# Kernel optimization log

Measured on AMD Instinct MI355X. Metric: run time of the kernel, lower is better.

Reference implementation:

```python
import jax, jax.numpy as jnp
import numpy as np

# NF4 codebook (bitsandbytes values)
NF4_LEVELS = jnp.array([-1.0, -0.6961928009986877, -0.5250730514526367, -0.39491748809814453,
                        -0.28444138169288635, -0.18477343022823334, -0.09105003625154495, 0.0,
                        0.07958029955625534, 0.16093020141124725, 0.24611230194568634,
                        0.33791524171829224, 0.44070982933044434, 0.5626170039176941,
                        0.7229568362236023, 1.0], dtype=jnp.float32)

IN_FEATURES = 4096
OUT_FEATURES = 4096


def setup_inputs() -> dict:
    key = jax.random.key(0)
    k1, k2, k3, k4 = jax.random.split(key, 4)
    x = jax.random.normal(k1, (4, 2048, IN_FEATURES), dtype=jnp.float32)
    # packed uint8 bytes (stored as int32 in [0,256)), shape (O, I//2)
    packed = jax.random.randint(k2, (OUT_FEATURES, IN_FEATURES // 2), 0, 256, dtype=jnp.int32)
    absmax = jax.random.uniform(k3, (OUT_FEATURES,), dtype=jnp.float32) + 1e-3
    bias = jax.random.normal(k4, (OUT_FEATURES,), dtype=jnp.float32)
    return {"x": x, "packed": packed, "absmax": absmax, "bias": bias}


def dequantize_nf4(packed, absmax):
    # packed: (O, I//2) int bytes; high nibble first, then low nibble
    high = (packed >> 4) & 15
    low = packed & 15
    idx = jnp.stack([high, low], axis=2).reshape(packed.shape[0], -1)  # (O, I)
    w = NF4_LEVELS[idx]                    # LUT dequant, (O, I)
    return w * absmax[:, None]             # per-row absmax scaling


def reference(x, packed, absmax, bias):
    # forward: dequantize weight on-the-fly, then F.linear(x, W, bias)
    w = dequantize_nf4(packed, absmax)     # (O, I)
    return jnp.einsum('bsi,oi->bso', x, w) + bias
```

## Files before the change

### kernel.cpp

```cpp
#include <hip/hip_runtime.h>
#include <hip/hip_bf16.h>
#include <stdint.h>

#define M_DIM 8192
#define N_DIM 4096
#define K_DIM 4096

typedef __bf16 bf16_t;
typedef __attribute__((ext_vector_type(8))) __bf16 bf16x8;
typedef __attribute__((ext_vector_type(4))) __bf16 bf16x4;
typedef __attribute__((ext_vector_type(4))) float f32x4;
typedef __attribute__((ext_vector_type(16))) float f32x16;

__constant__ float NF4_LUT[16] = {
    -1.0f, -0.6961928009986877f, -0.5250730514526367f, -0.39491748809814453f,
    -0.28444138169288635f, -0.18477343022823334f, -0.09105003625154495f, 0.0f,
    0.07958029955625534f, 0.16093020141124725f, 0.24611230194568634f,
    0.33791524171829224f, 0.44070982933044434f, 0.5626170039176941f,
    0.7229568362236023f, 1.0f};

__global__ __launch_bounds__(256) void dequant_nf4_kernel(
    const int* __restrict__ packed, const float* __restrict__ absmax,
    bf16_t* __restrict__ W) {
  const int t = blockIdx.x * 256 + threadIdx.x;
  const int row = t >> 9;
  const int c = t & 511;
  const int lane = threadIdx.x & 63;
  const int lutbits = __float_as_int(NF4_LUT[lane & 15]);

  const int4 p = ((const int4*)packed)[t];
  const float am = absmax[row];
  bf16x8 v;
#pragma unroll
  for (int q = 0; q < 4; ++q) {
    const int byte = (q == 0 ? p.x : q == 1 ? p.y : q == 2 ? p.z : p.w) & 255;
    const float hi =
        __int_as_float(__builtin_amdgcn_ds_bpermute(((byte >> 4) & 15) << 2, lutbits));
    const float lo =
        __int_as_float(__builtin_amdgcn_ds_bpermute((byte & 15) << 2, lutbits));
    v[2 * q] = (bf16_t)(hi * am);
    v[2 * q + 1] = (bf16_t)(lo * am);
  }
  *((bf16x8*)&W[(size_t)row * K_DIM + c * 8]) = v;
}

__global__ __launch_bounds__(256) void cvt_bf16_kernel(
    const float* __restrict__ x, bf16_t* __restrict__ y) {
  const int t = blockIdx.x * 256 + threadIdx.x;
  const float4 a = ((const float4*)x)[t];
  bf16x4 v;
  v[0] = (bf16_t)a.x; v[1] = (bf16_t)a.y; v[2] = (bf16_t)a.z; v[3] = (bf16_t)a.w;
  *((bf16x4*)&y[(size_t)t * 4]) = v;
}

#define GLD_LDS16(g, l)                                                     \
  __builtin_amdgcn_global_load_lds(                                        \
      (const __attribute__((address_space(1))) void*)(g),                   \
      (__attribute__((address_space(3))) void*)(l), 16, 0, 0)

#define MFMA32(a, b, c) \
  __builtin_amdgcn_mfma_f32_32x32x16_bf16((a), (b), (c), 0, 0, 0)

#define STAGE_A1(tt, lds)                                    \
  do {                                                       \
    GLD_LDS16(gA1a + (size_t)(tt) * 64, (lds) + dA0);        \
    GLD_LDS16(gA1b + (size_t)(tt) * 64, (lds) + dA0 + 16384);\
  } while (0)
#define STAGE_A2(tt, lds)                                    \
  do {                                                       \
    GLD_LDS16(gA2a + (size_t)(tt) * 64, (lds) + dA0 + 8192); \
    GLD_LDS16(gA2b + (size_t)(tt) * 64, (lds) + dA0 + 24576);\
  } while (0)
#define STAGE_B1(tt, lds)                                    \
  do {                                                       \
    GLD_LDS16(gB1a + (size_t)(tt) * 64, (lds) + dB0);        \
    GLD_LDS16(gB1b + (size_t)(tt) * 64, (lds) + dB0 + 16384);\
  } while (0)
#define STAGE_B2(tt, lds)                                    \
  do {                                                       \
    GLD_LDS16(gB2a + (size_t)(tt) * 64, (lds) + dB0 + 4096); \
    GLD_LDS16(gB2b + (size_t)(tt) * 64, (lds) + dB0 + 20480);\
  } while (0)

#define END_BARRIER()                \
  asm volatile("" ::: "memory");     \
  __builtin_amdgcn_s_barrier();      \
  asm volatile("" ::: "memory")

#define MID_BARRIER()                                   \
  asm volatile("" ::: "memory");                        \
  __builtin_amdgcn_s_barrier();                         \
  asm volatile("s_waitcnt lgkmcnt(0)" ::: "memory");    \
  __builtin_amdgcn_sched_barrier(0)

__global__ __launch_bounds__(512, 2) void gemm_nf4_kernel(
    const bf16_t* __restrict__ A, const bf16_t* __restrict__ B,
    const float* __restrict__ bias, float* __restrict__ C) {
  constexpr int NT = K_DIM / 64;
  __shared__ __align__(16) bf16_t sA[2][256 * 64];
  __shared__ __align__(16) bf16_t sB[2][256 * 64];

  const int tid = threadIdx.x;
  const int wave = tid >> 6, lane = tid & 63;
  const int wm = wave >> 2, wn = wave & 3;
  const int l31 = lane & 31, hi = lane >> 5, l7 = lane & 7;

  const int id = (blockIdx.x & 7) * 64 + (blockIdx.x >> 3);
  const int blockM = (id & 31) * 256;
  const int blockN = (id >> 5) * 256;

  const int rqa = tid >> 3;
  const int cira = ((tid & 7) ^ (rqa & 7)) * 8;
  const bf16_t* gA1a = A + (size_t)(blockM + rqa) * K_DIM + cira;
  const bf16_t* gA1b = gA1a + (size_t)128 * K_DIM;
  const bf16_t* gA2a = gA1a + (size_t)64 * K_DIM;
  const bf16_t* gA2b = gA1a + (size_t)192 * K_DIM;
  const int s0 = tid >> 8, cis = tid & 255;
  const int rqb = cis >> 3;
  const int cirb = ((cis & 7) ^ (rqb & 7)) * 8;
  const bf16_t* gB1a = B + (size_t)(blockN + s0 * 64 + rqb) * K_DIM + cirb;
  const bf16_t* gB1b = gB1a + (size_t)128 * K_DIM;
  const bf16_t* gB2a = gB1a + (size_t)32 * K_DIM;
  const bf16_t* gB2b = gB1a + (size_t)160 * K_DIM;
  const int dA0 = tid * 16;
  const int dB0 = s0 * 8192 + cis * 16;

  const int aBase = (wm * 128 + l31) * 128;
  const int bBase = (wn * 64 + l31) * 128;
  int cOff[4];
#pragma unroll
  for (int ks = 0; ks < 4; ++ks) cOff[ks] = ((ks * 2 + hi) ^ l7) * 16;

  f32x16 acc[4][2];
#pragma unroll
  for (int i = 0; i < 4; ++i)
#pragma unroll
    for (int j = 0; j < 2; ++j) acc[i][j] = (f32x16)(0.0f);

  {
    char* sa0 = (char*)sA[0];
    char* sb0 = (char*)sB[0];
    char* sa1 = (char*)sA[1];
    char* sb1 = (char*)sB[1];
    STAGE_A1(0, sa0);
    STAGE_B1(0, sb0);
    STAGE_A2(0, sa0);
    STAGE_B2(0, sb0);
    STAGE_A1(1, sa1);
    STAGE_B1(1, sb1);
    asm volatile("s_waitcnt vmcnt(4)" ::: "memory");
    __builtin_amdgcn_s_barrier();
    asm volatile("" ::: "memory");
  }

  for (int t = 0; t < NT; ++t) {
    char* sa = (char*)sA[t & 1];
    char* sao = (char*)sA[(t + 1) & 1];
    char* sb = (char*)sB[t & 1];
    char* sbo = (char*)sB[(t + 1) & 1];

    bf16x8 af[2][4], bq[2][4];

#pragma unroll
    for (int mt = 0; mt < 2; ++mt)
#pragma unroll
      for (int ks = 0; ks < 4; ++ks)
        af[mt][ks] = *(const bf16x8*)(sa + aBase + mt * 4096 + cOff[ks]);
#pragma unroll
    for (int nt = 0; nt < 2; ++nt)
#pragma unroll
      for (int ks = 0; ks < 4; ++ks)
        bq[nt][ks] = *(const bf16x8*)(sb + bBase + nt * 4096 + cOff[ks]);
    if (t + 1 < NT) {
      STAGE_A2(t + 1, sao);
      STAGE_B2(t + 1, sbo);
    }
    asm volatile("s_waitcnt lgkmcnt(8)" ::: "memory");
    MID_BARRIER();
    __builtin_amdgcn_s_setprio(1);
#pragma unroll
    for (int ks = 0; ks < 4; ++ks)
#pragma unroll
      for (int mt = 0; mt < 2; ++mt)
#pragma unroll
        for (int nt = 0; nt < 2; ++nt)
          acc[mt][nt] = MFMA32(af[mt][ks], bq[nt][ks], acc[mt][nt]);
    __builtin_amdgcn_s_setprio(0);
    END_BARRIER();

#pragma unroll
    for (int mt = 0; mt < 2; ++mt)
#pragma unroll
      for (int ks = 0; ks < 4; ++ks)
        af[mt][ks] = *(const bf16x8*)(sa + aBase + 8192 + mt * 4096 + cOff[ks]);
    if (t + 2 < NT) {
      STAGE_A1(t + 2, sa);
      STAGE_B1(t + 2, sb);
    }
    MID_BARRIER();
    __builtin_amdgcn_s_setprio(1);
#pragma unroll
    for (int ks = 0; ks < 4; ++ks)
#pragma unroll
      for (int mt = 0; mt < 2; ++mt)
#pragma unroll
        for (int nt = 0; nt < 2; ++nt)
          acc[2 + mt][nt] = MFMA32(af[mt][ks], bq[nt][ks], acc[2 + mt][nt]);
    __builtin_amdgcn_s_setprio(0);
    if (t < NT - 2)
      asm volatile("s_waitcnt vmcnt(4)" ::: "memory");
    else
      asm volatile("s_waitcnt vmcnt(0)" ::: "memory");
    END_BARRIER();
  }

#pragma unroll
  for (int nt = 0; nt < 2; ++nt) {
    const int n = blockN + wn * 64 + nt * 32 + l31;
    const float bv = bias[n];
#pragma unroll
    for (int mt = 0; mt < 4; ++mt) {
      const int mbase = blockM + wm * 128 + mt * 32 + hi * 4;
      f32x16 v = acc[mt][nt];
#pragma unroll
      for (int r = 0; r < 16; ++r) {
        const int m = mbase + (r & 3) + 8 * (r >> 2);
        C[(size_t)m * N_DIM + n] = v[r] + bv;
      }
    }
  }
}

__global__ __launch_bounds__(256) void fallback_kernel(
    const float* __restrict__ x, const int* __restrict__ packed,
    const float* __restrict__ absmax, const float* __restrict__ bias,
    float* __restrict__ out) {
  const int idx = blockIdx.x * 256 + threadIdx.x;
  const int m = idx / N_DIM, n = idx % N_DIM;
  const int* prow = packed + (size_t)n * (K_DIM / 2);
  const float* xr = x + (size_t)m * K_DIM;
  float s = 0.0f;
  for (int p = 0; p < K_DIM / 2; ++p) {
    const int b = prow[p] & 255;
    s += xr[2 * p] * NF4_LUT[(b >> 4) & 15] + xr[2 * p + 1] * NF4_LUT[b & 15];
  }
  out[idx] = s * absmax[n] + bias[n];
}

extern "C" void kernel_launch(void* const* d_in, const int* in_sizes, int n_in,
                              void* d_out, int out_size, void* d_ws,
                              size_t ws_size, hipStream_t stream) {
  const float* x = (const float*)d_in[0];
  const int* packed = (const int*)d_in[1];
  const float* absmax = (const float*)d_in[2];
  const float* bias = (const float*)d_in[3];
  float* out = (float*)d_out;

  const size_t wBytes = (size_t)N_DIM * K_DIM * sizeof(bf16_t);
  const size_t xBytes = (size_t)M_DIM * K_DIM * sizeof(bf16_t);
  if (ws_size < wBytes + xBytes) {
    fallback_kernel<<<dim3((M_DIM * N_DIM) / 256), dim3(256), 0, stream>>>(
        x, packed, absmax, bias, out);
    return;
  }

  bf16_t* W = (bf16_t*)d_ws;
  bf16_t* xb = (bf16_t*)((char*)d_ws + wBytes);

  dequant_nf4_kernel<<<dim3((N_DIM * (K_DIM / 2) / 4) / 256), dim3(256), 0,
                       stream>>>(packed, absmax, W);
  cvt_bf16_kernel<<<dim3((M_DIM * K_DIM / 4) / 256), dim3(256), 0, stream>>>(
      x, xb);
  gemm_nf4_kernel<<<dim3((M_DIM / 256) * (N_DIM / 256)), dim3(512), 0,
                    stream>>>(xb, W, bias, out);
}
```

Measured before the change: 521.4 us.

## Switch GEMM to 16x16x32 MFMA, drop mid barriers, merge prep kernels

The GEMM inner loop now uses 16x16x32 bf16 MFMA tiles with 8x4 accumulators per wave instead of 32x32x16, with new LDS read offsets and epilogue indexing. One of the two block barriers per half-iteration is removed and replaced with an lgkmcnt(0) fence. The dequant and x-conversion kernels are merged into one launch to save a kernel launch. Removing barriers risks races on the double-buffered LDS, and smaller MFMA tiles need more instructions for the same work.

```diff
diff --git a/kernel.cpp b/kernel.cpp
--- a/kernel.cpp
+++ b/kernel.cpp
@@ -10,7 +10,6 @@
 typedef __attribute__((ext_vector_type(8))) __bf16 bf16x8;
 typedef __attribute__((ext_vector_type(4))) __bf16 bf16x4;
 typedef __attribute__((ext_vector_type(4))) float f32x4;
-typedef __attribute__((ext_vector_type(16))) float f32x16;
 
 __constant__ float NF4_LUT[16] = {
     -1.0f, -0.6961928009986877f, -0.5250730514526367f, -0.39491748809814453f,
@@ -19,38 +18,42 @@
     0.33791524171829224f, 0.44070982933044434f, 0.5626170039176941f,
     0.7229568362236023f, 1.0f};
 
-__global__ __launch_bounds__(256) void dequant_nf4_kernel(
+#define DQ_BLOCKS ((N_DIM * (K_DIM / 2) / 4) / 256)
+#define CVT_BLOCKS ((M_DIM * K_DIM / 4) / 256)
+
+__global__ __launch_bounds__(256) void prep_kernel(
     const int* __restrict__ packed, const float* __restrict__ absmax,
-    bf16_t* __restrict__ W) {
-  const int t = blockIdx.x * 256 + threadIdx.x;
-  const int row = t >> 9;
-  const int c = t & 511;
-  const int lane = threadIdx.x & 63;
-  const int lutbits = __float_as_int(NF4_LUT[lane & 15]);
-
-  const int4 p = ((const int4*)packed)[t];
-  const float am = absmax[row];
-  bf16x8 v;
-#pragma unroll
-  for (int q = 0; q < 4; ++q) {
-    const int byte = (q == 0 ? p.x : q == 1 ? p.y : q == 2 ? p.z : p.w) & 255;
-    const float hi =
-        __int_as_float(__builtin_amdgcn_ds_bpermute(((byte >> 4) & 15) << 2, lutbits));
-    const float lo =
-        __int_as_float(__builtin_amdgcn_ds_bpermute((byte & 15) << 2, lutbits));
-    v[2 * q] = (bf16_t)(hi * am);
-    v[2 * q + 1] = (bf16_t)(lo * am);
-  }
-  *((bf16x8*)&W[(size_t)row * K_DIM + c * 8]) = v;
-}
-
-__global__ __launch_bounds__(256) void cvt_bf16_kernel(
-    const float* __restrict__ x, bf16_t* __restrict__ y) {
-  const int t = blockIdx.x * 256 + threadIdx.x;
-  const float4 a = ((const float4*)x)[t];
-  bf16x4 v;
-  v[0] = (bf16_t)a.x; v[1] = (bf16_t)a.y; v[2] = (bf16_t)a.z; v[3] = (bf16_t)a.w;
-  *((bf16x4*)&y[(size_t)t * 4]) = v;
+    bf16_t* __restrict__ W, const float* __restrict__ x,
+    bf16_t* __restrict__ y) {
+  if (blockIdx.x < DQ_BLOCKS) {
+    const int t = blockIdx.x * 256 + threadIdx.x;
+    const int row = t >> 9;
+    const int c = t & 511;
+    const int lane = threadIdx.x & 63;
+    const int lutbits = __float_as_int(NF4_LUT[lane & 15]);
+
+    const int4 p = ((const int4*)packed)[t];
+    const float am = absmax[row];
+    bf16x8 v;
+#pragma unroll
+    for (int q = 0; q < 4; ++q) {
+      const int byte = (q == 0 ? p.x : q == 1 ? p.y : q == 2 ? p.z : p.w) & 255;
+      const float hi = __int_as_float(
+          __builtin_amdgcn_ds_bpermute(((byte >> 4) & 15) << 2, lutbits));
+      const float lo = __int_as_float(
+          __builtin_amdgcn_ds_bpermute((byte & 15) << 2, lutbits));
+      v[2 * q] = (bf16_t)(hi * am);
+      v[2 * q + 1] = (bf16_t)(lo * am);
+    }
+    *((bf16x8*)&W[(size_t)row * K_DIM + c * 8]) = v;
+  } else {
+    const int t = (blockIdx.x - DQ_BLOCKS) * 256 + threadIdx.x;
+    const float4 a = ((const float4*)x)[t];
+    bf16x4 v;
+    v[0] = (bf16_t)a.x; v[1] = (bf16_t)a.y;
+    v[2] = (bf16_t)a.z; v[3] = (bf16_t)a.w;
+    *((bf16x4*)&y[(size_t)t * 4]) = v;
+  }
 }
 
 #define GLD_LDS16(g, l)                                                     \
@@ -58,8 +61,8 @@
       (const __attribute__((address_space(1))) void*)(g),                   \
       (__attribute__((address_space(3))) void*)(l), 16, 0, 0)
 
-#define MFMA32(a, b, c) \
-  __builtin_amdgcn_mfma_f32_32x32x16_bf16((a), (b), (c), 0, 0, 0)
+#define MFMA16(a, b, c) \
+  __builtin_amdgcn_mfma_f32_16x16x32_bf16((a), (b), (c), 0, 0, 0)
 
 #define STAGE_A1(tt, lds)                                    \
   do {                                                       \
@@ -82,14 +85,12 @@
     GLD_LDS16(gB2b + (size_t)(tt) * 64, (lds) + dB0 + 20480);\
   } while (0)
 
-#define END_BARRIER()                \
+#define BARRIER()                    \
   asm volatile("" ::: "memory");     \
   __builtin_amdgcn_s_barrier();      \
   asm volatile("" ::: "memory")
 
-#define MID_BARRIER()                                   \
-  asm volatile("" ::: "memory");                        \
-  __builtin_amdgcn_s_barrier();                         \
+#define LGKM0_FENCE()                                   \
   asm volatile("s_waitcnt lgkmcnt(0)" ::: "memory");    \
   __builtin_amdgcn_sched_barrier(0)
 
@@ -103,7 +104,7 @@
   const int tid = threadIdx.x;
   const int wave = tid >> 6, lane = tid & 63;
   const int wm = wave >> 2, wn = wave & 3;
-  const int l31 = lane & 31, hi = lane >> 5, l7 = lane & 7;
+  const int quad = lane >> 4, l15 = lane & 15, l7 = lane & 7;
 
   const int id = (blockIdx.x & 7) * 64 + (blockIdx.x >> 3);
   const int blockM = (id & 31) * 256;
@@ -125,17 +126,16 @@
   const int dA0 = tid * 16;
   const int dB0 = s0 * 8192 + cis * 16;
 
-  const int aBase = (wm * 128 + l31) * 128;
-  const int bBase = (wn * 64 + l31) * 128;
-  int cOff[4];
-#pragma unroll
-  for (int ks = 0; ks < 4; ++ks) cOff[ks] = ((ks * 2 + hi) ^ l7) * 16;
-
-  f32x16 acc[4][2];
-#pragma unroll
-  for (int i = 0; i < 4; ++i)
-#pragma unroll
-    for (int j = 0; j < 2; ++j) acc[i][j] = (f32x16)(0.0f);
+  const int aBase = (wm * 128 + l15) * 128;
+  const int bBase = (wn * 64 + l15) * 128;
+  const int sl0 = (quad ^ l7) * 16;
+  const int sl1 = ((4 | quad) ^ l7) * 16;
+
+  f32x4 acc[8][4];
+#pragma unroll
+  for (int i = 0; i < 8; ++i)
+#pragma unroll
+    for (int j = 0; j < 4; ++j) acc[i][j] = (f32x4)(0.0f);
 
   {
     char* sa0 = (char*)sA[0];
@@ -159,74 +159,72 @@
     char* sb = (char*)sB[t & 1];
     char* sbo = (char*)sB[(t + 1) & 1];
 
-    bf16x8 af[2][4], bq[2][4];
-
-#pragma unroll
-    for (int mt = 0; mt < 2; ++mt)
-#pragma unroll
-      for (int ks = 0; ks < 4; ++ks)
-        af[mt][ks] = *(const bf16x8*)(sa + aBase + mt * 4096 + cOff[ks]);
-#pragma unroll
-    for (int nt = 0; nt < 2; ++nt)
-#pragma unroll
-      for (int ks = 0; ks < 4; ++ks)
-        bq[nt][ks] = *(const bf16x8*)(sb + bBase + nt * 4096 + cOff[ks]);
+    bf16x8 af[4][2], bq[4][2];
+
+#pragma unroll
+    for (int i = 0; i < 4; ++i) {
+      af[i][0] = *(const bf16x8*)(sa + aBase + i * 2048 + sl0);
+      af[i][1] = *(const bf16x8*)(sa + aBase + i * 2048 + sl1);
+    }
+#pragma unroll
+    for (int j = 0; j < 4; ++j) {
+      bq[j][0] = *(const bf16x8*)(sb + bBase + j * 2048 + sl0);
+      bq[j][1] = *(const bf16x8*)(sb + bBase + j * 2048 + sl1);
+    }
     if (t + 1 < NT) {
       STAGE_A2(t + 1, sao);
       STAGE_B2(t + 1, sbo);
     }
-    asm volatile("s_waitcnt lgkmcnt(8)" ::: "memory");
-    MID_BARRIER();
+    BARRIER();
+    LGKM0_FENCE();
     __builtin_amdgcn_s_setprio(1);
 #pragma unroll
-    for (int ks = 0; ks < 4; ++ks)
-#pragma unroll
-      for (int mt = 0; mt < 2; ++mt)
-#pragma unroll
-        for (int nt = 0; nt < 2; ++nt)
-          acc[mt][nt] = MFMA32(af[mt][ks], bq[nt][ks], acc[mt][nt]);
+    for (int i = 0; i < 4; ++i)
+#pragma unroll
+      for (int j = 0; j < 4; ++j) {
+        acc[i][j] = MFMA16(af[i][0], bq[j][0], acc[i][j]);
+        acc[i][j] = MFMA16(af[i][1], bq[j][1], acc[i][j]);
+      }
     __builtin_amdgcn_s_setprio(0);
-    END_BARRIER();
-
-#pragma unroll
-    for (int mt = 0; mt < 2; ++mt)
-#pragma unroll
-      for (int ks = 0; ks < 4; ++ks)
-        af[mt][ks] = *(const bf16x8*)(sa + aBase + 8192 + mt * 4096 + cOff[ks]);
+
+#pragma unroll
+    for (int i = 0; i < 4; ++i) {
+      af[i][0] = *(const bf16x8*)(sa + aBase + 8192 + i * 2048 + sl0);
+      af[i][1] = *(const bf16x8*)(sa + aBase + 8192 + i * 2048 + sl1);
+    }
     if (t + 2 < NT) {
       STAGE_A1(t + 2, sa);
       STAGE_B1(t + 2, sb);
     }
-    MID_BARRIER();
+    LGKM0_FENCE();
     __builtin_amdgcn_s_setprio(1);
 #pragma unroll
-    for (int ks = 0; ks < 4; ++ks)
-#pragma unroll
-      for (int mt = 0; mt < 2; ++mt)
-#pragma unroll
-        for (int nt = 0; nt < 2; ++nt)
-          acc[2 + mt][nt] = MFMA32(af[mt][ks], bq[nt][ks], acc[2 + mt][nt]);
+    for (int i = 0; i < 4; ++i)
+#pragma unroll
+      for (int j = 0; j < 4; ++j) {
+        acc[4 + i][j] = MFMA16(af[i][0], bq[j][0], acc[4 + i][j]);
+        acc[4 + i][j] = MFMA16(af[i][1], bq[j][1], acc[4 + i][j]);
+      }
     __builtin_amdgcn_s_setprio(0);
     if (t < NT - 2)
       asm volatile("s_waitcnt vmcnt(4)" ::: "memory");
     else
       asm volatile("s_waitcnt vmcnt(0)" ::: "memory");
-    END_BARRIER();
-  }
-
-#pragma unroll
-  for (int nt = 0; nt < 2; ++nt) {
-    const int n = blockN + wn * 64 + nt * 32 + l31;
+    BARRIER();
+  }
+
+#pragma unroll
+  for (int j = 0; j < 4; ++j) {
+    const int n = blockN + wn * 64 + j * 16 + l15;
     const float bv = bias[n];
 #pragma unroll
-    for (int mt = 0; mt < 4; ++mt) {
-      const int mbase = blockM + wm * 128 + mt * 32 + hi * 4;
-      f32x16 v = acc[mt][nt];
-#pragma unroll
-      for (int r = 0; r < 16; ++r) {
-        const int m = mbase + (r & 3) + 8 * (r >> 2);
-        C[(size_t)m * N_DIM + n] = v[r] + bv;
-      }
+    for (int i = 0; i < 8; ++i) {
+      const int m0 = blockM + wm * 128 + i * 16 + quad * 4;
+      f32x4 v = acc[i][j];
+      C[(size_t)(m0 + 0) * N_DIM + n] = v[0] + bv;
+      C[(size_t)(m0 + 1) * N_DIM + n] = v[1] + bv;
+      C[(size_t)(m0 + 2) * N_DIM + n] = v[2] + bv;
+      C[(size_t)(m0 + 3) * N_DIM + n] = v[3] + bv;
     }
   }
 }
@@ -267,10 +265,8 @@
   bf16_t* W = (bf16_t*)d_ws;
   bf16_t* xb = (bf16_t*)((char*)d_ws + wBytes);
 
-  dequant_nf4_kernel<<<dim3((N_DIM * (K_DIM / 2) / 4) / 256), dim3(256), 0,
-                       stream>>>(packed, absmax, W);
-  cvt_bf16_kernel<<<dim3((M_DIM * K_DIM / 4) / 256), dim3(256), 0, stream>>>(
-      x, xb);
+  prep_kernel<<<dim3(DQ_BLOCKS + CVT_BLOCKS), dim3(256), 0, stream>>>(
+      packed, absmax, W, x, xb);
   gemm_nf4_kernel<<<dim3((M_DIM / 256) * (N_DIM / 256)), dim3(512), 0,
                     stream>>>(xb, W, bias, out);
 }
```

New measurement: 479.6 us. -8.0%, faster.
